# Performance work log

Hardware: AMD Instinct MI355X
Metric: run time of the kernel (lower is better)

Reference implementation:

```python
import jax, jax.numpy as jnp
import numpy as np

N1, N2, N3, N4, N5 = 1_000_000, 131_072, 16_384, 2_048, 256
C = 48  # plane_cls


def setup_inputs() -> dict:
    key = jax.random.key(0)
    ks = jax.random.split(key, 10)
    return {
        "slabel": jax.random.normal(ks[0], (N1, C), dtype=jnp.float32),
        "parent2": jax.random.randint(ks[1], (N1,), 0, N2, dtype=jnp.int32),
        "parent3": jax.random.randint(ks[2], (N2,), 0, N3, dtype=jnp.int32),
        "parent4": jax.random.randint(ks[3], (N3,), 0, N4, dtype=jnp.int32),
        "parent5": jax.random.randint(ks[4], (N4,), 0, N5, dtype=jnp.int32),
        "idx2": jax.random.randint(ks[5], (N1,), 0, N2, dtype=jnp.int32),
        "idx3": jax.random.randint(ks[6], (N1,), 0, N3, dtype=jnp.int32),
        "idx4": jax.random.randint(ks[7], (N1,), 0, N4, dtype=jnp.int32),
        "idx5": jax.random.randint(ks[8], (N1,), 0, N5, dtype=jnp.int32),
    }


def reference(slabel, parent2, parent3, parent4, parent5, idx2, idx3, idx4, idx5):
    # Each stride-2 MinkowskiConvolution with per-offset identity kernels is a
    # sum of child voxel features into the parent voxel: a segment_sum over the
    # sparse-conv kernel map (here given as parent index arrays).
    f2 = jax.ops.segment_sum(slabel, parent2, num_segments=N2)  # [N2, C]
    f3 = jax.ops.segment_sum(f2, parent3, num_segments=N3)      # [N3, C]
    f4 = jax.ops.segment_sum(f3, parent4, num_segments=N4)      # [N4, C]
    f5 = jax.ops.segment_sum(f4, parent5, num_segments=N5)      # [N5, C]
    # Gather per-query-point features at each level, then argmax over classes.
    s2 = jnp.argmax(f2[idx2], axis=-1)
    s3 = jnp.argmax(f3[idx3], axis=-1)
    s4 = jnp.argmax(f4[idx4], axis=-1)
    s5 = jnp.argmax(f5[idx5], axis=-1)
    return (s2, s3, s4, s5)
```

## Files before the change

kernel.cpp:

```cpp
#include <hip/hip_runtime.h>

#define N1 1000000
#define N2 131072
#define N3 16384
#define N4 2048
#define N5 256
#define C 48
#define CAP 48

#define ZDW ((N3 + N4 + N5) * C)
#define ZF4 (ZDW / 4)
#define ZBLK ((ZF4 + 255) / 256)
__global__ void reorder_zero_kernel(const int* __restrict__ parent,
                                    int* __restrict__ cnt,
                                    int* __restrict__ rowid,
                                    float4* __restrict__ ftab) {
    if ((int)blockIdx.x < ZBLK) {
        int i = blockIdx.x * 256 + threadIdx.x;
        if (i < ZF4) ftab[i] = make_float4(0.f, 0.f, 0.f, 0.f);
        return;
    }
    int i = ((int)blockIdx.x - ZBLK) * 256 + threadIdx.x;
    if (i >= N1) return;
    int p = parent[i];
    int s = atomicAdd(&cnt[p], 1);
    if (s < CAP) rowid[p * CAP + s] = i;
}

__global__ void segsum_fused_kernel(const float* __restrict__ src,
                                    const int* __restrict__ rowid,
                                    const int* __restrict__ cnt,
                                    const int* __restrict__ parent3,
                                    float* __restrict__ f3,
                                    unsigned char* __restrict__ tab2, int nseg) {
    int wid = threadIdx.x >> 6;
    int lane = threadIdx.x & 63;
    int seg = blockIdx.x * 4 + wid;
    if (seg >= nseg) return;
    int n = cnt[seg];
    if (n > CAP) n = CAP;
    int rv = (lane < 16 && lane < n) ? rowid[seg * CAP + lane] : 0;
    if (n > 16) {
        if (lane >= 16 && lane < n) rv = rowid[seg * CAP + lane];
    }
    int g = lane / 12;
    int c4 = lane - g * 12;
    const bool act = (lane < 60);
    float4 acc = make_float4(0.f, 0.f, 0.f, 0.f);
    for (int k = 0; k < n; k += 15) {
        int r0 = __shfl(rv, k + g);
        int r1 = __shfl(rv, k + 5 + g);
        int r2 = __shfl(rv, k + 10 + g);
        bool p0 = act && (k + g < n);
        bool p1 = act && (k + 5 + g < n);
        bool p2 = act && (k + 10 + g < n);
        float4 v0 = p0 ? *(const float4*)(src + (size_t)r0 * C + c4 * 4)
                       : make_float4(0.f, 0.f, 0.f, 0.f);
        float4 v1 = p1 ? *(const float4*)(src + (size_t)r1 * C + c4 * 4)
                       : make_float4(0.f, 0.f, 0.f, 0.f);
        float4 v2 = p2 ? *(const float4*)(src + (size_t)r2 * C + c4 * 4)
                       : make_float4(0.f, 0.f, 0.f, 0.f);
        acc.x += v0.x + v1.x + v2.x;
        acc.y += v0.y + v1.y + v2.y;
        acc.z += v0.z + v1.z + v2.z;
        acc.w += v0.w + v1.w + v2.w;
    }
    float4 tot = acc;
#pragma unroll
    for (int gg = 1; gg < 5; ++gg) {
        int sl = c4 + 12 * gg;
        tot.x += __shfl(acc.x, sl);
        tot.y += __shfl(acc.y, sl);
        tot.z += __shfl(acc.z, sl);
        tot.w += __shfl(acc.w, sl);
    }
    int q = lane >> 2;
    float vx = __shfl(tot.x, q);
    float vy = __shfl(tot.y, q);
    float vz = __shfl(tot.z, q);
    float vw = __shfl(tot.w, q);
    int m = lane & 3;
    float val = (m == 0) ? vx : (m == 1) ? vy : (m == 2) ? vz : vw;
    int p3 = parent3[seg];
    const bool ch = (lane < C);
    if (ch) atomicAdd(&f3[(size_t)p3 * C + lane], val);
    float bv = ch ? val : -__builtin_inff();
    int bi = ch ? lane : 0x7fffffff;
#pragma unroll
    for (int d = 32; d > 0; d >>= 1) {
        float ov = __shfl_xor(bv, d);
        int oi = __shfl_xor(bi, d);
        if (ov > bv || (ov == bv && oi < bi)) { bv = ov; bi = oi; }
    }
    if (lane == 0) tab2[seg] = (unsigned char)bi;
}

__device__ __forceinline__ int argmax48(const float4* __restrict__ row) {
    float best = -__builtin_inff();
    int bi = 0;
#pragma unroll
    for (int i = 0; i < 12; ++i) {
        float4 v = row[i];
        if (v.x > best) { best = v.x; bi = 4 * i + 0; }
        if (v.y > best) { best = v.y; bi = 4 * i + 1; }
        if (v.z > best) { best = v.z; bi = 4 * i + 2; }
        if (v.w > best) { best = v.w; bi = 4 * i + 3; }
    }
    return bi;
}

__global__ void level_kernel(const float* __restrict__ fsrc,
                             const int* __restrict__ parent,
                             float* __restrict__ fdst,
                             unsigned char* __restrict__ tabsrc,
                             int nrows, int nblkA) {
    if ((int)blockIdx.x < nblkA) {
        int e = blockIdx.x * 256 + threadIdx.x;
        if (e < nrows * C) {
            unsigned r = (unsigned)e / C;
            unsigned c = (unsigned)e - r * C;
            atomicAdd(&fdst[(unsigned)parent[r] * C + c], fsrc[e]);
        }
    } else {
        int r = (blockIdx.x - nblkA) * 256 + threadIdx.x;
        if (r < nrows) tabsrc[r] = (unsigned char)argmax48((const float4*)fsrc + r * 12);
    }
}

__global__ void final_kernel(const unsigned char* __restrict__ tab2,
                             const unsigned char* __restrict__ tab3,
                             const unsigned char* __restrict__ tab4,
                             const float4* __restrict__ f5,
                             const int4* __restrict__ idx2,
                             const int4* __restrict__ idx3,
                             const int4* __restrict__ idx4,
                             const int4* __restrict__ idx5,
                             int4* __restrict__ out) {
    __shared__ unsigned char t5[N5];
    int tid = threadIdx.x;
    t5[tid] = (unsigned char)argmax48(f5 + tid * 12);
    __syncthreads();
    const int NQ = N1 / 4;
    int t = blockIdx.x * blockDim.x + tid;
    if (t >= NQ) return;
    int4 a = idx2[t], b = idx3[t], c = idx4[t], d = idx5[t];
    out[t] = make_int4(tab2[a.x], tab2[a.y], tab2[a.z], tab2[a.w]);
    out[NQ + t] = make_int4(tab3[b.x], tab3[b.y], tab3[b.z], tab3[b.w]);
    out[2 * NQ + t] = make_int4(tab4[c.x], tab4[c.y], tab4[c.z], tab4[c.w]);
    out[3 * NQ + t] = make_int4(t5[d.x], t5[d.y], t5[d.z], t5[d.w]);
}

extern "C" void kernel_launch(void* const* d_in, const int* in_sizes, int n_in,
                              void* d_out, int out_size, void* d_ws, size_t ws_size,
                              hipStream_t stream) {
    const float* slabel  = (const float*)d_in[0];
    const int* parent2   = (const int*)d_in[1];
    const int* parent3   = (const int*)d_in[2];
    const int* parent4   = (const int*)d_in[3];
    const int* parent5   = (const int*)d_in[4];
    const int* idx2      = (const int*)d_in[5];
    const int* idx3      = (const int*)d_in[6];
    const int* idx4      = (const int*)d_in[7];
    const int* idx5      = (const int*)d_in[8];
    int* out = (int*)d_out;

    float* f3 = (float*)d_ws;
    float* f4 = f3 + (size_t)N3 * C;
    float* f5 = f4 + (size_t)N4 * C;
    int* cnt2 = (int*)(f5 + (size_t)N5 * C);
    int* rowid2 = cnt2 + N2;
    unsigned char* tab2 = (unsigned char*)(rowid2 + (size_t)N2 * CAP);
    unsigned char* tab3 = tab2 + N2;
    unsigned char* tab4 = tab3 + N3;

    hipMemsetAsync(cnt2, 0, (size_t)N2 * 4, stream);

    reorder_zero_kernel<<<ZBLK + (N1 + 255) / 256, 256, 0, stream>>>(
        parent2, cnt2, rowid2, (float4*)d_ws);

    segsum_fused_kernel<<<N2 / 4, 256, 0, stream>>>(
        slabel, rowid2, cnt2, parent3, f3, tab2, N2);

    level_kernel<<<3072 + 64, 256, 0, stream>>>(f3, parent4, f4, tab3, N3, 3072);

    level_kernel<<<384 + 8, 256, 0, stream>>>(f4, parent5, f5, tab4, N4, 384);

    final_kernel<<<(N1 / 4 + 255) / 256, 256, 0, stream>>>(
        tab2, tab3, tab4, (const float4*)f5,
        (const int4*)idx2, (const int4*)idx3, (const int4*)idx4, (const int4*)idx5,
        (int4*)out);
}
```

Baseline: 162.5 us.

## Replace atomic level kernels with gather-based fused tail using child lists

Builds child index lists for levels 4 and 5 in the setup kernel, then computes f4, tab4, f5 and tab3 in one tail kernel by gathering from f3 instead of doing atomic scatter-adds over two separate launches. This removes one launch and the f4/f5 zeroing and atomic traffic. It also lowers the level-2 child capacity from 48 to 32. That risks dropping children when a parent has more than 32 (expected count is about 7.6, so unlikely), and the level-4 capacity of 64 is similarly assumed sufficient. The tail kernel's f5 blocks each walk about 64 f3 rows serially per wave, which may be latency-bound.

```diff
diff --git a/kernel.cpp b/kernel.cpp
--- a/kernel.cpp
+++ b/kernel.cpp
@@ -6,25 +6,49 @@
 #define N4 2048
 #define N5 256
 #define C 48
-#define CAP 48
-
-#define ZDW ((N3 + N4 + N5) * C)
-#define ZF4 (ZDW / 4)
-#define ZBLK ((ZF4 + 255) / 256)
-__global__ void reorder_zero_kernel(const int* __restrict__ parent,
-                                    int* __restrict__ cnt,
-                                    int* __restrict__ rowid,
-                                    float4* __restrict__ ftab) {
-    if ((int)blockIdx.x < ZBLK) {
-        int i = blockIdx.x * 256 + threadIdx.x;
-        if (i < ZF4) ftab[i] = make_float4(0.f, 0.f, 0.f, 0.f);
-        return;
-    }
-    int i = ((int)blockIdx.x - ZBLK) * 256 + threadIdx.x;
-    if (i >= N1) return;
-    int p = parent[i];
-    int s = atomicAdd(&cnt[p], 1);
-    if (s < CAP) rowid[p * CAP + s] = i;
+#define CAP 32
+#define CAP4 64
+#define CAP5 64
+
+#define ZF4 ((N3 * C) / 4)
+#define ZBLK (ZF4 / 256)
+#define SBLK ((N1 + 255) / 256)
+#define I4BLK (N3 / 256)
+#define I5BLK (N4 / 256)
+__global__ void setup_kernel(const int* __restrict__ parent2,
+                             const int* __restrict__ parent4,
+                             const int* __restrict__ parent5,
+                             int* __restrict__ cnt2, int* __restrict__ rowid,
+                             int* __restrict__ cnt4, int* __restrict__ kid4,
+                             int* __restrict__ cnt5, int* __restrict__ kid5,
+                             float4* __restrict__ f3z) {
+    int b = (int)blockIdx.x;
+    if (b < ZBLK) {
+        f3z[b * 256 + threadIdx.x] = make_float4(0.f, 0.f, 0.f, 0.f);
+        return;
+    }
+    b -= ZBLK;
+    if (b < SBLK) {
+        int i = b * 256 + threadIdx.x;
+        if (i >= N1) return;
+        int p = parent2[i];
+        int s = atomicAdd(&cnt2[p], 1);
+        if (s < CAP) rowid[p * CAP + s] = i;
+        return;
+    }
+    b -= SBLK;
+    if (b < I4BLK) {
+        int r3 = b * 256 + threadIdx.x;
+        int r4 = parent4[r3];
+        int s = atomicAdd(&cnt4[r4], 1);
+        if (s < CAP4) kid4[r4 * CAP4 + s] = r3;
+        return;
+    }
+    b -= I4BLK;
+    int r4 = b * 256 + threadIdx.x;
+    int r5 = parent5[r4];
+    int s = atomicAdd(&cnt5[r5], 1);
+    if (s < CAP5) kid5[r5 * CAP5 + s] = r4;
 }
 
 __global__ void segsum_fused_kernel(const float* __restrict__ src,
@@ -109,22 +133,50 @@
     return bi;
 }
 
-__global__ void level_kernel(const float* __restrict__ fsrc,
-                             const int* __restrict__ parent,
-                             float* __restrict__ fdst,
-                             unsigned char* __restrict__ tabsrc,
-                             int nrows, int nblkA) {
-    if ((int)blockIdx.x < nblkA) {
-        int e = blockIdx.x * 256 + threadIdx.x;
-        if (e < nrows * C) {
-            unsigned r = (unsigned)e / C;
-            unsigned c = (unsigned)e - r * C;
-            atomicAdd(&fdst[(unsigned)parent[r] * C + c], fsrc[e]);
+__global__ void tail_kernel(const float* __restrict__ f3,
+                            const int* __restrict__ cnt4, const int* __restrict__ kid4,
+                            const int* __restrict__ cnt5, const int* __restrict__ kid5,
+                            float* __restrict__ f5,
+                            unsigned char* __restrict__ tab3,
+                            unsigned char* __restrict__ tab4) {
+    int b = (int)blockIdx.x;
+    if (b >= N5) {
+        int r = (b - N5) * 256 + threadIdx.x;
+        tab3[r] = (unsigned char)argmax48((const float4*)f3 + r * 12);
+        return;
+    }
+    __shared__ float f5part[4][C];
+    int wid = threadIdx.x >> 6;
+    int lane = threadIdx.x & 63;
+    const bool ch = (lane < C);
+    int m5 = cnt5[b];
+    if (m5 > CAP5) m5 = CAP5;
+    float wacc = 0.f;
+    for (int j = wid; j < m5; j += 4) {
+        int r4 = kid5[b * CAP5 + j];
+        int m4 = cnt4[r4];
+        if (m4 > CAP4) m4 = CAP4;
+        float facc = 0.f;
+        for (int s = 0; s < m4; ++s) {
+            int r3 = kid4[r4 * CAP4 + s];
+            if (ch) facc += f3[(size_t)r3 * C + lane];
         }
-    } else {
-        int r = (blockIdx.x - nblkA) * 256 + threadIdx.x;
-        if (r < nrows) tabsrc[r] = (unsigned char)argmax48((const float4*)fsrc + r * 12);
-    }
+        float bv = ch ? facc : -__builtin_inff();
+        int bi = ch ? lane : 0x7fffffff;
+#pragma unroll
+        for (int d = 32; d > 0; d >>= 1) {
+            float ov = __shfl_xor(bv, d);
+            int oi = __shfl_xor(bi, d);
+            if (ov > bv || (ov == bv && oi < bi)) { bv = ov; bi = oi; }
+        }
+        if (lane == 0) tab4[r4] = (unsigned char)bi;
+        wacc += facc;
+    }
+    if (ch) f5part[wid][lane] = wacc;
+    __syncthreads();
+    int t = threadIdx.x;
+    if (t < C)
+        f5[(size_t)b * C + t] = f5part[0][t] + f5part[1][t] + f5part[2][t] + f5part[3][t];
 }
 
 __global__ void final_kernel(const unsigned char* __restrict__ tab2,
@@ -165,25 +217,28 @@
     int* out = (int*)d_out;
 
     float* f3 = (float*)d_ws;
-    float* f4 = f3 + (size_t)N3 * C;
-    float* f5 = f4 + (size_t)N4 * C;
-    int* cnt2 = (int*)(f5 + (size_t)N5 * C);
-    int* rowid2 = cnt2 + N2;
-    unsigned char* tab2 = (unsigned char*)(rowid2 + (size_t)N2 * CAP);
+    int* cnt2 = (int*)(f3 + (size_t)N3 * C);
+    int* cnt4 = cnt2 + N2;
+    int* cnt5 = cnt4 + N4;
+    float* f5 = (float*)(cnt5 + N5);
+    int* rowid2 = (int*)(f5 + (size_t)N5 * C);
+    int* kid4 = rowid2 + (size_t)N2 * CAP;
+    int* kid5 = kid4 + (size_t)N4 * CAP4;
+    unsigned char* tab2 = (unsigned char*)(kid5 + (size_t)N5 * CAP5);
     unsigned char* tab3 = tab2 + N2;
     unsigned char* tab4 = tab3 + N3;
 
-    hipMemsetAsync(cnt2, 0, (size_t)N2 * 4, stream);
-
-    reorder_zero_kernel<<<ZBLK + (N1 + 255) / 256, 256, 0, stream>>>(
-        parent2, cnt2, rowid2, (float4*)d_ws);
+    hipMemsetAsync(cnt2, 0, (size_t)(N2 + N4 + N5) * 4, stream);
+
+    setup_kernel<<<ZBLK + SBLK + I4BLK + I5BLK, 256, 0, stream>>>(
+        parent2, parent4, parent5, cnt2, rowid2, cnt4, kid4, cnt5, kid5,
+        (float4*)f3);
 
     segsum_fused_kernel<<<N2 / 4, 256, 0, stream>>>(
         slabel, rowid2, cnt2, parent3, f3, tab2, N2);
 
-    level_kernel<<<3072 + 64, 256, 0, stream>>>(f3, parent4, f4, tab3, N3, 3072);
-
-    level_kernel<<<384 + 8, 256, 0, stream>>>(f4, parent5, f5, tab4, N4, 384);
+    tail_kernel<<<N5 + N3 / 256, 256, 0, stream>>>(
+        f3, cnt4, kid4, cnt5, kid5, f5, tab3, tab4);
 
     final_kernel<<<(N1 / 4 + 255) / 256, 256, 0, stream>>>(
         tab2, tab3, tab4, (const float4*)f5,
```

New measurement: 189.9 us. 1.17x slower.

## Fuse level-4 and level-5 scatters and move level-4 argmax into final kernel

Applied to the files above, without the earlier changes.

The two per-level scatter kernels become one kernel. It adds each f3 element into f4 and, through the composed parent chain parent5[parent4[r]], directly into f5, which removes one launch and one serialization point. The level-4 argmax table is now built in shared memory by every block of the final kernel. That kernel runs as a fixed 256-block grid-stride loop. The per-parent row capacity also drops from 48 to 32, which shrinks the rowid buffer but silently drops children beyond 32. The trade-offs are heavier atomic contention on the small f5 array and redundant argmax work over f4 in every final block.

```diff
diff --git a/kernel.cpp b/kernel.cpp
--- a/kernel.cpp
+++ b/kernel.cpp
@@ -6,24 +6,25 @@
 #define N4 2048
 #define N5 256
 #define C 48
-#define CAP 48
+#define CAP 32
 
-#define ZDW ((N3 + N4 + N5) * C)
-#define ZF4 (ZDW / 4)
+#define ZF4 (((N3 + N4 + N5) * C) / 4)
 #define ZBLK ((ZF4 + 255) / 256)
-__global__ void reorder_zero_kernel(const int* __restrict__ parent,
-                                    int* __restrict__ cnt,
-                                    int* __restrict__ rowid,
-                                    float4* __restrict__ ftab) {
-    if ((int)blockIdx.x < ZBLK) {
-        int i = blockIdx.x * 256 + threadIdx.x;
+#define SBLK ((N1 + 255) / 256)
+__global__ void setup_kernel(const int* __restrict__ parent2,
+                             int* __restrict__ cnt2, int* __restrict__ rowid,
+                             float4* __restrict__ ftab) {
+    int b = (int)blockIdx.x;
+    if (b < ZBLK) {
+        int i = b * 256 + threadIdx.x;
         if (i < ZF4) ftab[i] = make_float4(0.f, 0.f, 0.f, 0.f);
         return;
     }
-    int i = ((int)blockIdx.x - ZBLK) * 256 + threadIdx.x;
+    b -= ZBLK;
+    int i = b * 256 + threadIdx.x;
     if (i >= N1) return;
-    int p = parent[i];
-    int s = atomicAdd(&cnt[p], 1);
+    int p = parent2[i];
+    int s = atomicAdd(&cnt2[p], 1);
     if (s < CAP) rowid[p * CAP + s] = i;
 }
 
@@ -109,45 +110,51 @@
     return bi;
 }
 
-__global__ void level_kernel(const float* __restrict__ fsrc,
-                             const int* __restrict__ parent,
-                             float* __restrict__ fdst,
-                             unsigned char* __restrict__ tabsrc,
-                             int nrows, int nblkA) {
-    if ((int)blockIdx.x < nblkA) {
-        int e = blockIdx.x * 256 + threadIdx.x;
-        if (e < nrows * C) {
-            unsigned r = (unsigned)e / C;
-            unsigned c = (unsigned)e - r * C;
-            atomicAdd(&fdst[(unsigned)parent[r] * C + c], fsrc[e]);
-        }
+__global__ void level34_kernel(const float* __restrict__ f3,
+                               const int* __restrict__ parent4,
+                               const int* __restrict__ parent5,
+                               float* __restrict__ f4,
+                               float* __restrict__ f5,
+                               unsigned char* __restrict__ tab3) {
+    int b = (int)blockIdx.x;
+    if (b < 3072) {
+        int e = b * 256 + threadIdx.x;
+        unsigned r = (unsigned)e / C;
+        unsigned c = (unsigned)e - r * C;
+        float v = f3[e];
+        int r4 = parent4[r];
+        atomicAdd(&f4[(size_t)r4 * C + c], v);
+        int r5 = parent5[r4];
+        atomicAdd(&f5[(size_t)r5 * C + c], v);
     } else {
-        int r = (blockIdx.x - nblkA) * 256 + threadIdx.x;
-        if (r < nrows) tabsrc[r] = (unsigned char)argmax48((const float4*)fsrc + r * 12);
+        int r = (b - 3072) * 256 + threadIdx.x;
+        tab3[r] = (unsigned char)argmax48((const float4*)f3 + r * 12);
     }
 }
 
 __global__ void final_kernel(const unsigned char* __restrict__ tab2,
                              const unsigned char* __restrict__ tab3,
-                             const unsigned char* __restrict__ tab4,
+                             const float4* __restrict__ f4,
                              const float4* __restrict__ f5,
                              const int4* __restrict__ idx2,
                              const int4* __restrict__ idx3,
                              const int4* __restrict__ idx4,
                              const int4* __restrict__ idx5,
                              int4* __restrict__ out) {
+    __shared__ unsigned char t4[N4];
     __shared__ unsigned char t5[N5];
-    int tid = threadIdx.x;
-    t5[tid] = (unsigned char)argmax48(f5 + tid * 12);
+    for (int r = threadIdx.x; r < N4; r += 256)
+        t4[r] = (unsigned char)argmax48(f4 + r * 12);
+    t5[threadIdx.x] = (unsigned char)argmax48(f5 + threadIdx.x * 12);
     __syncthreads();
     const int NQ = N1 / 4;
-    int t = blockIdx.x * blockDim.x + tid;
-    if (t >= NQ) return;
-    int4 a = idx2[t], b = idx3[t], c = idx4[t], d = idx5[t];
-    out[t] = make_int4(tab2[a.x], tab2[a.y], tab2[a.z], tab2[a.w]);
-    out[NQ + t] = make_int4(tab3[b.x], tab3[b.y], tab3[b.z], tab3[b.w]);
-    out[2 * NQ + t] = make_int4(tab4[c.x], tab4[c.y], tab4[c.z], tab4[c.w]);
-    out[3 * NQ + t] = make_int4(t5[d.x], t5[d.y], t5[d.z], t5[d.w]);
+    for (int t = blockIdx.x * 256 + threadIdx.x; t < NQ; t += gridDim.x * 256) {
+        int4 a = idx2[t], b = idx3[t], c = idx4[t], d = idx5[t];
+        out[t]          = make_int4(tab2[a.x], tab2[a.y], tab2[a.z], tab2[a.w]);
+        out[NQ + t]     = make_int4(tab3[b.x], tab3[b.y], tab3[b.z], tab3[b.w]);
+        out[2 * NQ + t] = make_int4(t4[c.x], t4[c.y], t4[c.z], t4[c.w]);
+        out[3 * NQ + t] = make_int4(t5[d.x], t5[d.y], t5[d.z], t5[d.w]);
+    }
 }
 
 extern "C" void kernel_launch(void* const* d_in, const int* in_sizes, int n_in,
@@ -171,22 +178,20 @@
     int* rowid2 = cnt2 + N2;
     unsigned char* tab2 = (unsigned char*)(rowid2 + (size_t)N2 * CAP);
     unsigned char* tab3 = tab2 + N2;
-    unsigned char* tab4 = tab3 + N3;
 
     hipMemsetAsync(cnt2, 0, (size_t)N2 * 4, stream);
 
-    reorder_zero_kernel<<<ZBLK + (N1 + 255) / 256, 256, 0, stream>>>(
+    setup_kernel<<<ZBLK + SBLK, 256, 0, stream>>>(
         parent2, cnt2, rowid2, (float4*)d_ws);
 
     segsum_fused_kernel<<<N2 / 4, 256, 0, stream>>>(
         slabel, rowid2, cnt2, parent3, f3, tab2, N2);
 
-    level_kernel<<<3072 + 64, 256, 0, stream>>>(f3, parent4, f4, tab3, N3, 3072);
+    level34_kernel<<<3072 + 64, 256, 0, stream>>>(
+        f3, parent4, parent5, f4, f5, tab3);
 
-    level_kernel<<<384 + 8, 256, 0, stream>>>(f4, parent5, f5, tab4, N4, 384);
-
-    final_kernel<<<(N1 / 4 + 255) / 256, 256, 0, stream>>>(
-        tab2, tab3, tab4, (const float4*)f5,
+    final_kernel<<<256, 256, 0, stream>>>(
+        tab2, tab3, (const float4*)f4, (const float4*)f5,
         (const int4*)idx2, (const int4*)idx3, (const int4*)idx4, (const int4*)idx5,
         (int4*)out);
 }
```

After: 172.0 us. 1.06x slower.
